# Kernel optimization log

Hardware: AMD Instinct MI355X
Metric: run time of the kernel (lower is better)

The kernel has to match this reference:

```python
import jax, jax.numpy as jnp
import numpy as np

N = 50000   # nodes
E = 800000  # edges before self-loops
H = 4       # heads
D = 64      # num_h_feats (per-head out dim of hidden layers)
C = 2       # num_classes
NEG = 0.2   # DGL GATConv leaky_relu negative_slope
EPS = 1e-5  # BatchNorm eps


def setup_inputs() -> dict:
    key = jax.random.key(0)
    ks = jax.random.split(key, 16)
    inp = {}
    inp['feats'] = jax.random.normal(ks[0], (N, 9), jnp.float32)
    inp['W1'] = jax.random.normal(ks[1], (9, H * D), jnp.float32) * 0.1
    inp['al1'] = jax.random.normal(ks[2], (H, D), jnp.float32) * 0.1
    inp['ar1'] = jax.random.normal(ks[3], (H, D), jnp.float32) * 0.1
    inp['b1'] = jnp.zeros((H, D), jnp.float32)
    inp['Wm'] = jax.random.normal(ks[4], (D, H * D), jnp.float32) * 0.1
    inp['alm'] = jax.random.normal(ks[5], (H, D), jnp.float32) * 0.1
    inp['arm'] = jax.random.normal(ks[6], (H, D), jnp.float32) * 0.1
    inp['bm'] = jnp.zeros((H, D), jnp.float32)
    inp['W2'] = jax.random.normal(ks[7], (D, H * C), jnp.float32) * 0.1
    inp['al2'] = jax.random.normal(ks[8], (H, C), jnp.float32) * 0.1
    inp['ar2'] = jax.random.normal(ks[9], (H, C), jnp.float32) * 0.1
    inp['b2'] = jnp.zeros((H, C), jnp.float32)
    inp['gamma'] = jnp.ones((D,), jnp.float32)
    inp['beta'] = jnp.zeros((D,), jnp.float32)
    inp['src'] = jax.random.randint(ks[10], (E,), 0, N, jnp.int32)
    inp['dst'] = jax.random.randint(ks[11], (E,), 0, N, jnp.int32)
    return inp


def gat_layer(x, W, al, ar, b, src, dst, out_d):
    """DGL GATConv: linear -> per-edge attention -> dst-softmax -> scatter-sum."""
    n = x.shape[0]
    z = (x @ W).reshape(n, H, out_d)                 # [N, H, Dout]
    el = jnp.sum(z * al, axis=-1)                    # [N, H] attn on src
    er = jnp.sum(z * ar, axis=-1)                    # [N, H] attn on dst
    e = jax.nn.leaky_relu(el[src] + er[dst], NEG)    # [E, H]
    m = jax.ops.segment_max(e, dst, num_segments=n)  # per-dst max (stable softmax)
    a = jnp.exp(e - m[dst])
    s = jax.ops.segment_sum(a, dst, num_segments=n)
    alpha = a / s[dst]                               # [E, H]
    out = jax.ops.segment_sum(alpha[:, :, None] * z[src], dst, num_segments=n)
    return out + b                                   # [N, H, Dout]


def batchnorm(h, gamma, beta):
    mu = jnp.mean(h, axis=0)
    var = jnp.var(h, axis=0)
    return (h - mu) * jax.lax.rsqrt(var + EPS) * gamma + beta


def reference(feats, W1, al1, ar1, b1, Wm, alm, arm, bm, W2, al2, ar2, b2,
              gamma, beta, src, dst):
    # dgl.add_self_loop
    loop = jnp.arange(N, dtype=src.dtype)
    s = jnp.concatenate([src, loop])
    d = jnp.concatenate([dst, loop])
    h = gat_layer(feats, W1, al1, ar1, b1, s, d, D).sum(axis=1)  # head-sum
    h = batchnorm(h, gamma, beta)
    h = gat_layer(h, Wm, alm, arm, bm, s, d, D).sum(axis=1)
    h = batchnorm(h, gamma, beta)
    o = gat_layer(h, W2, al2, ar2, b2, s, d, C).sum(axis=1)      # [N, C]
    return o
```

## Files before the change

kernel.cpp:

```cpp
#include <hip/hip_runtime.h>
#include <hip/hip_bf16.h>

typedef __hip_bfloat16 bf16;
typedef __bf16 bf16x8 __attribute__((ext_vector_type(8)));
typedef float f32x4 __attribute__((ext_vector_type(4)));
typedef _Float16 h16;
typedef _Float16 h16x4 __attribute__((ext_vector_type(4)));

#define LOG2E 1.44269504088896340736f

__device__ __forceinline__ float b2f(bf16 v) { return __bfloat162float(v); }

__device__ __forceinline__ float ldin(const void* p, size_t i, int isb) {
    return isb ? b2f(((const bf16*)p)[i]) : ((const float*)p)[i];
}
__device__ __forceinline__ unsigned short f2bfbits(float f) {
    bf16 v = __float2bfloat16(f);
    return *(unsigned short*)&v;
}

__global__ __launch_bounds__(256) void prep_kernel(
    const void* __restrict__ feats, const void* __restrict__ W1, const void* __restrict__ Wm,
    const void* __restrict__ al1, const void* __restrict__ ar1,
    const void* __restrict__ alm, const void* __restrict__ arm,
    const unsigned* __restrict__ gbits,
    const int* __restrict__ dstv, int* __restrict__ deg,
    unsigned short* __restrict__ fpad, unsigned short* __restrict__ W1T,
    unsigned short* __restrict__ WmT,
    float* __restrict__ alf1, float* __restrict__ arf1,
    float* __restrict__ alfm, float* __restrict__ arfm,
    unsigned short* __restrict__ zhs, float* __restrict__ zcs, float* __restrict__ elp,
    int* __restrict__ flag, int Nn, int E) {
    int isb = (gbits[0] == 0x3F803F80u) ? 1 : 0;
    long t = (long)blockIdx.x * 256 + threadIdx.x;
    if (t == 0) *flag = isb;
    long b0 = (long)Nn * 8;
    long b1 = b0 + 2048;
    long b2 = b1 + 2048;
    long b3 = b2 + 256;
    long b4 = b3 + 268;
    long b5 = b4 + E;
    if (t < b0) {
        int s = (int)(t & 7); long n = t >> 3;
        int k0 = s * 8;
        union { unsigned short us[8]; uint4 v; } o;
#pragma unroll
        for (int j = 0; j < 8; j++) {
            int k = k0 + j;
            o.us[j] = (k < 9) ? f2bfbits(ldin(feats, (size_t)n * 9 + k, isb))
                              : (unsigned short)0;
        }
        *(uint4*)(fpad + t * 8) = o.v;
    } else if (t < b1) {
        long u = t - b0;
        int col = (int)(u >> 3), k0 = ((int)u & 7) * 8;
        union { unsigned short us[8]; uint4 v; } o;
#pragma unroll
        for (int j = 0; j < 8; j++) {
            int k = k0 + j;
            o.us[j] = (k < 9) ? f2bfbits(ldin(W1, (size_t)k * 256 + col, isb))
                              : (unsigned short)0;
        }
        *(uint4*)(W1T + u * 8) = o.v;
    } else if (t < b2) {
        long u = t - b1;
        int col = (int)(u >> 3), k0 = ((int)u & 7) * 8;
        union { unsigned short us[8]; uint4 v; } o;
#pragma unroll
        for (int j = 0; j < 8; j++) {
            int k = k0 + j;
            o.us[j] = f2bfbits(ldin(Wm, (size_t)k * 256 + col, isb));
        }
        *(uint4*)(WmT + u * 8) = o.v;
    } else if (t < b3) {
        int u = (int)(t - b2);
        alf1[u] = ldin(al1, u, isb) * LOG2E; arf1[u] = ldin(ar1, u, isb) * LOG2E;
        alfm[u] = ldin(alm, u, isb) * LOG2E; arfm[u] = ldin(arm, u, isb) * LOG2E;
    } else if (t < b4) {
        long u = t - b3;
        if (u < 4) {
            elp[(size_t)Nn * 4 + u] = -1e30f;
        } else if (u < 260) {
            zhs[(size_t)Nn * 256 + (u - 4)] = 0;
        } else {
            zcs[(size_t)Nn * 8 + (u - 260)] = 0.f;
        }
    } else if (t < b5) {
        atomicAdd(&deg[dstv[t - b4]], 1);
    }
}

__global__ __launch_bounds__(256) void scan1_kernel(
    const int* __restrict__ deg, int* __restrict__ off, int* __restrict__ bsum, int Nn) {
    __shared__ int s[256];
    int t = threadIdx.x, i = blockIdx.x * 256 + t;
    int v = (i < Nn) ? ((deg[i] + 3) & ~3) : 0;
    s[t] = v; __syncthreads();
#pragma unroll
    for (int o = 1; o < 256; o <<= 1) {
        int a = (t >= o) ? s[t - o] : 0;
        __syncthreads();
        s[t] += a;
        __syncthreads();
    }
    if (i < Nn) off[i] = s[t];
    if (t == 255) bsum[blockIdx.x] = s[255];
}

__global__ __launch_bounds__(256) void scan3_kernel(
    const int* __restrict__ deg, int* __restrict__ off, int* __restrict__ cur,
    int* __restrict__ adj, const int* __restrict__ bsum, int Nn, int NB) {
    __shared__ int s[256];
    int t = threadIdx.x;
    int v = (t < NB) ? bsum[t] : 0;
    s[t] = v; __syncthreads();
#pragma unroll
    for (int o = 1; o < 256; o <<= 1) {
        int a = (t >= o) ? s[t - o] : 0;
        __syncthreads();
        s[t] += a;
        __syncthreads();
    }
    s[t] -= v;
    __syncthreads();
    int base = s[blockIdx.x];
    int i = blockIdx.x * 256 + t;
    if (i < Nn) {
        int d = deg[i], pd = (d + 3) & ~3;
        int ex = off[i] - pd + base;
        off[i] = ex;
        cur[i] = ex;
        for (int j = d; j < pd; j++) adj[ex + j] = Nn;
        if (i == Nn - 1) {
            int tot = ex + pd;
            off[Nn] = tot;
            for (int j = 0; j < 32; j++) adj[tot + j] = Nn;
        }
    }
}

__global__ __launch_bounds__(256) void scatter_kernel(
    const int* __restrict__ src, const int* __restrict__ dst,
    int* __restrict__ cur, int* __restrict__ adj, int E) {
    int t = blockIdx.x * 256 + threadIdx.x;
    if (t < E) {
        int p = atomicAdd(&cur[dst[t]], 1);
        adj[p] = src[t];
    }
}

__global__ __launch_bounds__(256) void lin_mfma_l1_kernel(
    const unsigned short* __restrict__ xb, const unsigned short* __restrict__ WT,
    const float* __restrict__ alf, const float* __restrict__ arf,
    h16* __restrict__ zh, float* __restrict__ el, float* __restrict__ er, int Nn) {
    __shared__ h16 zs[16 * 256];
    int w = threadIdx.x >> 6;
    int l = threadIdx.x & 63;
    int quad = l >> 4, lc = l & 15;
    int node0 = blockIdx.x * 16;

    int mrow = node0 + lc; if (mrow >= Nn) mrow = Nn - 1;
    const bf16x8* xa = (const bf16x8*)(xb + (size_t)mrow * 64);
    bf16x8 a0 = xa[quad];
    bf16x8 a1 = xa[quad + 4];

    float pe[4] = {0.f, 0.f, 0.f, 0.f}, pr[4] = {0.f, 0.f, 0.f, 0.f};
    int row0 = quad * 4;
#pragma unroll
    for (int ct = 0; ct < 4; ++ct) {
        int col = w * 64 + ct * 16 + lc;
        const bf16x8* wb = (const bf16x8*)(WT + (size_t)col * 64);
        bf16x8 b0 = wb[quad];
        bf16x8 b1 = wb[quad + 4];
        f32x4 c = {0.f, 0.f, 0.f, 0.f};
        c = __builtin_amdgcn_mfma_f32_16x16x32_bf16(a0, b0, c, 0, 0, 0);
        c = __builtin_amdgcn_mfma_f32_16x16x32_bf16(a1, b1, c, 0, 0, 0);
        float av = alf[col], rv = arf[col];
#pragma unroll
        for (int r = 0; r < 4; ++r) {
            pe[r] = fmaf(c[r], av, pe[r]);
            pr[r] = fmaf(c[r], rv, pr[r]);
            zs[(row0 + r) * 256 + col] = (h16)c[r];
        }
    }
#pragma unroll
    for (int o = 1; o < 16; o <<= 1) {
#pragma unroll
        for (int r = 0; r < 4; ++r) {
            pe[r] += __shfl_xor(pe[r], o);
            pr[r] += __shfl_xor(pr[r], o);
        }
    }
    if (lc == 0) {
#pragma unroll
        for (int r = 0; r < 4; ++r) {
            int n = node0 + row0 + r;
            if (n < Nn) { el[n * 4 + w] = pe[r]; er[n * 4 + w] = pr[r]; }
        }
    }
    __syncthreads();
#pragma unroll
    for (int it = 0; it < 2; ++it) {
        int flat = it * 2048 + threadIdx.x * 8;
        int row = flat >> 8;
        if (node0 + row < Nn)
            *(uint4*)(zh + (size_t)node0 * 256 + flat) = *(const uint4*)(zs + flat);
    }
}

__global__ __launch_bounds__(256) void lin_mfma_bn_kernel(
    const float* __restrict__ x,
    const float* __restrict__ bnsum, const float* __restrict__ bnsumsq,
    const void* __restrict__ gamma, const void* __restrict__ beta,
    const unsigned short* __restrict__ WT,
    const float* __restrict__ alf, const float* __restrict__ arf,
    h16* __restrict__ zh, float* __restrict__ el, float* __restrict__ er,
    const int* __restrict__ flag, int Nn) {
    __shared__ h16 zs[16 * 256];
    __shared__ __align__(16) float scs[64], shs[64];
    int tid = threadIdx.x;
    if (tid < 64) {
        int isb = *flag;
        float inv_n = 1.f / (float)Nn;
        float mu = bnsum[tid] * inv_n;
        float var = bnsumsq[tid] * inv_n - mu * mu;
        float s = rsqrtf(var + 1e-5f) * ldin(gamma, tid, isb);
        scs[tid] = s;
        shs[tid] = ldin(beta, tid, isb) - mu * s;
    }
    __syncthreads();

    int w = tid >> 6;
    int l = tid & 63;
    int quad = l >> 4, lc = l & 15;
    int node0 = blockIdx.x * 16;

    int mrow = node0 + lc; if (mrow >= Nn) mrow = Nn - 1;
    const float* xr = x + (size_t)mrow * 64 + quad * 8;
    float4 f0 = ((const float4*)xr)[0];
    float4 f1 = ((const float4*)xr)[1];
    float4 f2 = ((const float4*)(xr + 32))[0];
    float4 f3 = ((const float4*)(xr + 32))[1];
    float4 s0 = ((const float4*)(scs + quad * 8))[0];
    float4 s1 = ((const float4*)(scs + quad * 8))[1];
    float4 s2 = ((const float4*)(scs + 32 + quad * 8))[0];
    float4 s3 = ((const float4*)(scs + 32 + quad * 8))[1];
    float4 h0 = ((const float4*)(shs + quad * 8))[0];
    float4 h1 = ((const float4*)(shs + quad * 8))[1];
    float4 h2 = ((const float4*)(shs + 32 + quad * 8))[0];
    float4 h3 = ((const float4*)(shs + 32 + quad * 8))[1];

    union { bf16x8 v; unsigned short s[8]; } ua, ub;
    ua.s[0] = f2bfbits(fmaf(f0.x, s0.x, h0.x));
    ua.s[1] = f2bfbits(fmaf(f0.y, s0.y, h0.y));
    ua.s[2] = f2bfbits(fmaf(f0.z, s0.z, h0.z));
    ua.s[3] = f2bfbits(fmaf(f0.w, s0.w, h0.w));
    ua.s[4] = f2bfbits(fmaf(f1.x, s1.x, h1.x));
    ua.s[5] = f2bfbits(fmaf(f1.y, s1.y, h1.y));
    ua.s[6] = f2bfbits(fmaf(f1.z, s1.z, h1.z));
    ua.s[7] = f2bfbits(fmaf(f1.w, s1.w, h1.w));
    ub.s[0] = f2bfbits(fmaf(f2.x, s2.x, h2.x));
    ub.s[1] = f2bfbits(fmaf(f2.y, s2.y, h2.y));
    ub.s[2] = f2bfbits(fmaf(f2.z, s2.z, h2.z));
    ub.s[3] = f2bfbits(fmaf(f2.w, s2.w, h2.w));
    ub.s[4] = f2bfbits(fmaf(f3.x, s3.x, h3.x));
    ub.s[5] = f2bfbits(fmaf(f3.y, s3.y, h3.y));
    ub.s[6] = f2bfbits(fmaf(f3.z, s3.z, h3.z));
    ub.s[7] = f2bfbits(fmaf(f3.w, s3.w, h3.w));
    bf16x8 a0 = ua.v, a1 = ub.v;

    float pe[4] = {0.f, 0.f, 0.f, 0.f}, pr[4] = {0.f, 0.f, 0.f, 0.f};
    int row0 = quad * 4;
#pragma unroll
    for (int ct = 0; ct < 4; ++ct) {
        int col = w * 64 + ct * 16 + lc;
        const bf16x8* wb = (const bf16x8*)(WT + (size_t)col * 64);
        bf16x8 b0 = wb[quad];
        bf16x8 b1 = wb[quad + 4];
        f32x4 c = {0.f, 0.f, 0.f, 0.f};
        c = __builtin_amdgcn_mfma_f32_16x16x32_bf16(a0, b0, c, 0, 0, 0);
        c = __builtin_amdgcn_mfma_f32_16x16x32_bf16(a1, b1, c, 0, 0, 0);
        float av = alf[col], rv = arf[col];
#pragma unroll
        for (int r = 0; r < 4; ++r) {
            pe[r] = fmaf(c[r], av, pe[r]);
            pr[r] = fmaf(c[r], rv, pr[r]);
            zs[(row0 + r) * 256 + col] = (h16)c[r];
        }
    }
#pragma unroll
    for (int o = 1; o < 16; o <<= 1) {
#pragma unroll
        for (int r = 0; r < 4; ++r) {
            pe[r] += __shfl_xor(pe[r], o);
            pr[r] += __shfl_xor(pr[r], o);
        }
    }
    if (lc == 0) {
#pragma unroll
        for (int r = 0; r < 4; ++r) {
            int n = node0 + row0 + r;
            if (n < Nn) { el[n * 4 + w] = pe[r]; er[n * 4 + w] = pr[r]; }
        }
    }
    __syncthreads();
#pragma unroll
    for (int it = 0; it < 2; ++it) {
        int flat = it * 2048 + threadIdx.x * 8;
        int row = flat >> 8;
        if (node0 + row < Nn)
            *(uint4*)(zh + (size_t)node0 * 256 + flat) = *(const uint4*)(zs + flat);
    }
}

__global__ __launch_bounds__(256) void bnstats_kernel(
    const float* __restrict__ x, float* __restrict__ bnsum, float* __restrict__ bnsumsq,
    int Nn) {
    __shared__ float ssum[4][64], ssq[4][64];
    int tid = threadIdx.x;
    int d = tid & 63, r = tid >> 6;
    float s = 0.f, q = 0.f;
    int stride = gridDim.x * 4;
    for (int n = blockIdx.x * 4 + r; n < Nn; n += stride) {
        float v = x[(size_t)n * 64 + d];
        s += v;
        q = fmaf(v, v, q);
    }
    ssum[r][d] = s; ssq[r][d] = q;
    __syncthreads();
    if (tid < 64) {
        float ts = ssum[0][tid] + ssum[1][tid] + ssum[2][tid] + ssum[3][tid];
        float tq = ssq[0][tid] + ssq[1][tid] + ssq[2][tid] + ssq[3][tid];
        atomicAdd(&bnsum[tid], ts);
        atomicAdd(&bnsumsq[tid], tq);
    }
}

__global__ __launch_bounds__(256) void lin3_kernel(
    const float* __restrict__ x,
    const float* __restrict__ bnsum, const float* __restrict__ bnsumsq,
    const void* __restrict__ gamma, const void* __restrict__ beta,
    const void* __restrict__ W, const void* __restrict__ al, const void* __restrict__ ar,
    float* __restrict__ zc, float* __restrict__ el, float* __restrict__ er,
    const int* __restrict__ flag, int Nn) {
    __shared__ __align__(16) float scs[64], shs[64];
    int isb = *flag;
    int tid = threadIdx.x;
    if (tid < 64) {
        float inv_n = 1.f / (float)Nn;
        float mu = bnsum[tid] * inv_n;
        float var = bnsumsq[tid] * inv_n - mu * mu;
        float s = rsqrtf(var + 1e-5f) * ldin(gamma, tid, isb);
        scs[tid] = s;
        shs[tid] = ldin(beta, tid, isb) - mu * s;
    }
    __syncthreads();
    int t = blockIdx.x * 256 + tid;
    if (t >= Nn * 4) return;
    int n = t >> 2, h = t & 3;
    const float4* xr4 = (const float4*)(x + (size_t)n * 64);
    float a0 = 0.f, a1 = 0.f;
#pragma unroll 4
    for (int kk = 0; kk < 16; kk++) {
        float4 xv = xr4[kk];
        int k = kk * 4;
        float xn;
        xn = fmaf(xv.x, scs[k + 0], shs[k + 0]);
        a0 += xn * ldin(W, (k + 0) * 8 + h * 2, isb);
        a1 += xn * ldin(W, (k + 0) * 8 + h * 2 + 1, isb);
        xn = fmaf(xv.y, scs[k + 1], shs[k + 1]);
        a0 += xn * ldin(W, (k + 1) * 8 + h * 2, isb);
        a1 += xn * ldin(W, (k + 1) * 8 + h * 2 + 1, isb);
        xn = fmaf(xv.z, scs[k + 2], shs[k + 2]);
        a0 += xn * ldin(W, (k + 2) * 8 + h * 2, isb);
        a1 += xn * ldin(W, (k + 2) * 8 + h * 2 + 1, isb);
        xn = fmaf(xv.w, scs[k + 3], shs[k + 3]);
        a0 += xn * ldin(W, (k + 3) * 8 + h * 2, isb);
        a1 += xn * ldin(W, (k + 3) * 8 + h * 2 + 1, isb);
    }
    zc[n * 8 + h * 2 + 0] = a0;
    zc[n * 8 + h * 2 + 1] = a1;
    el[t] = (a0 * ldin(al, h * 2, isb) + a1 * ldin(al, h * 2 + 1, isb)) * LOG2E;
    er[t] = (a0 * ldin(ar, h * 2, isb) + a1 * ldin(ar, h * 2 + 1, isb)) * LOG2E;
}

#define GATH(ev, zv, sv)                                        \
    {                                                           \
        ev[0] = el[sv.x * 4 + h]; ev[1] = el[sv.y * 4 + h];     \
        ev[2] = el[sv.z * 4 + h]; ev[3] = el[sv.w * 4 + h];     \
        zv[0] = zrow[(size_t)sv.x * 64 + l];                    \
        zv[1] = zrow[(size_t)sv.y * 64 + l];                    \
        zv[2] = zrow[(size_t)sv.z * 64 + l];                    \
        zv[3] = zrow[(size_t)sv.w * 64 + l];                    \
    }
#define COMP(ev, zv)                                        \
    {                                                       \
        _Pragma("unroll") for (int j = 0; j < 4; j++) {     \
            float e = ev[j] + ern;                          \
            e = fmaxf(e, 0.2f * e);                         \
            float wj = __builtin_amdgcn_exp2f(e);           \
            lsum += wj;                                     \
            acc.x = fmaf(wj, (float)zv[j].x, acc.x);        \
            acc.y = fmaf(wj, (float)zv[j].y, acc.y);        \
            acc.z = fmaf(wj, (float)zv[j].z, acc.z);        \
            acc.w = fmaf(wj, (float)zv[j].w, acc.w);        \
        }                                                   \
    }

__global__ __launch_bounds__(256) void gat_agg64_kernel(
    const h16* __restrict__ zh, const float* __restrict__ el, const float* __restrict__ er,
    const int* __restrict__ off, const int* __restrict__ adj, const void* __restrict__ bias,
    float* __restrict__ x, const int* __restrict__ flag, int Nn, int total_waves) {
    int isb = *flag;
    int tid = threadIdx.x;
    int l = tid & 63;
    int h = l >> 4;
    int gw = blockIdx.x * 4 + (tid >> 6);
    const h16x4* zrow = (const h16x4*)zh;

    float4 bsl;
    bsl.x = ldin(bias, l * 4 + 0, isb);
    bsl.y = ldin(bias, l * 4 + 1, isb);
    bsl.z = ldin(bias, l * 4 + 2, isb);
    bsl.w = ldin(bias, l * 4 + 3, isb);

    if (gw >= Nn) return;

    int n = gw;
    int fs0 = off[n], fs1 = off[n + 1];
    float fel = el[n * 4 + h], fer = er[n * 4 + h];
    int4 fsv = *(const int4*)(adj + fs0);

    while (true) {
        int s0 = fs0;
        int nb = (fs1 - fs0) >> 2;
        float eln = fel, ern = fer;
        int4 svA = fsv;
        h16x4 zself = zrow[(size_t)n * 64 + l];
        int nn = n + total_waves;
        if (nn < Nn) {
            fs0 = off[nn]; fs1 = off[nn + 1];
            fel = el[nn * 4 + h]; fer = er[nn * 4 + h];
            fsv = *(const int4*)(adj + fs0);
        }

        float e0 = eln + ern;
        e0 = fmaxf(e0, 0.2f * e0);
        float w0 = __builtin_amdgcn_exp2f(e0);
        float lsum = w0;
        float4 acc = {0.f, 0.f, 0.f, 0.f};

        if (nb > 0) {
            float evA[4], evB[4], evC[4];
            h16x4 zvA[4], zvB[4], zvC[4];
            GATH(evA, zvA, svA);
            int4 svB = *(const int4*)(adj + s0 + 4);
            if (nb > 1) GATH(evB, zvB, svB);
            int4 svC = *(const int4*)(adj + s0 + 8);
            int k = 0;
            while (true) {
                if (k + 2 < nb) GATH(evC, zvC, svC);
                svA = *(const int4*)(adj + s0 + (k + 3) * 4);
                COMP(evA, zvA);
                if (++k >= nb) break;
                if (k + 2 < nb) GATH(evA, zvA, svA);
                svB = *(const int4*)(adj + s0 + (k + 3) * 4);
                COMP(evB, zvB);
                if (++k >= nb) break;
                if (k + 2 < nb) GATH(evB, zvB, svB);
                svC = *(const int4*)(adj + s0 + (k + 3) * 4);
                COMP(evC, zvC);
                if (++k >= nb) break;
            }
        }

        acc.x = fmaf(w0, (float)zself.x, acc.x);
        acc.y = fmaf(w0, (float)zself.y, acc.y);
        acc.z = fmaf(w0, (float)zself.z, acc.z);
        acc.w = fmaf(w0, (float)zself.w, acc.w);

        float inv = 1.f / lsum;
        float4 r;
        r.x = fmaf(acc.x, inv, bsl.x);
        r.y = fmaf(acc.y, inv, bsl.y);
        r.z = fmaf(acc.z, inv, bsl.z);
        r.w = fmaf(acc.w, inv, bsl.w);
#pragma unroll
        for (int o = 16; o < 64; o <<= 1) {
            r.x += __shfl_xor(r.x, o);
            r.y += __shfl_xor(r.y, o);
            r.z += __shfl_xor(r.z, o);
            r.w += __shfl_xor(r.w, o);
        }
        if (h == 0) ((float4*)(x + (size_t)n * 64))[l & 15] = r;
        if (nn >= Nn) break;
        n = nn;
    }
}
#undef GATH
#undef COMP

#define GATH2(ev, zv, sv)                                       \
    {                                                           \
        ev[0] = el[sv.x * 4 + h]; zv[0] = zc2[sv.x * 4 + h];    \
        ev[1] = el[sv.y * 4 + h]; zv[1] = zc2[sv.y * 4 + h];    \
        ev[2] = el[sv.z * 4 + h]; zv[2] = zc2[sv.z * 4 + h];    \
        ev[3] = el[sv.w * 4 + h]; zv[3] = zc2[sv.w * 4 + h];    \
    }
#define COMP2(ev, zv)                                       \
    {                                                       \
        _Pragma("unroll") for (int j = 0; j < 4; j++) {     \
            float e = ev[j] + er_nh;                        \
            e = fmaxf(e, 0.2f * e);                         \
            float w = __builtin_amdgcn_exp2f(e);            \
            lsum += w;                                      \
            a0 = fmaf(w, zv[j].x, a0);                      \
            a1 = fmaf(w, zv[j].y, a1);                      \
        }                                                   \
    }

__global__ __launch_bounds__(256) void gat_agg2_kernel(
    const float* __restrict__ zc, const float* __restrict__ el, const float* __restrict__ er,
    const int* __restrict__ off, const int* __restrict__ adj, const void* __restrict__ bias,
    void* __restrict__ out, const int* __restrict__ flag, int Nn) {
    int isb = *flag;
    int t = blockIdx.x * 256 + threadIdx.x;
    if (t >= Nn * 4) return;
    int n = t >> 2, h = t & 3;
    const float2* zc2 = (const float2*)zc;
    float er_nh = er[n * 4 + h];
    float e0 = el[n * 4 + h] + er_nh;
    e0 = fmaxf(e0, 0.2f * e0);
    float w0 = __builtin_amdgcn_exp2f(e0);
    float lsum = w0;
    float2 zn = zc2[n * 4 + h];
    float a0 = w0 * zn.x, a1 = w0 * zn.y;
    int s0 = off[n];
    int nb = (off[n + 1] - s0) >> 2;
    if (nb > 0) {
        float evA[4], evB[4], evC[4];
        float2 zvA[4], zvB[4], zvC[4];
        int4 svA = *(const int4*)(adj + s0);
        GATH2(evA, zvA, svA);
        int4 svB = *(const int4*)(adj + s0 + 4);
        if (nb > 1) GATH2(evB, zvB, svB);
        int4 svC = *(const int4*)(adj + s0 + 8);
        int k = 0;
        while (true) {
            if (k + 2 < nb) GATH2(evC, zvC, svC);
            svA = *(const int4*)(adj + s0 + (k + 3) * 4);
            COMP2(evA, zvA);
            if (++k >= nb) break;
            if (k + 2 < nb) GATH2(evA, zvA, svA);
            svB = *(const int4*)(adj + s0 + (k + 3) * 4);
            COMP2(evB, zvB);
            if (++k >= nb) break;
            if (k + 2 < nb) GATH2(evB, zvB, svB);
            svC = *(const int4*)(adj + s0 + (k + 3) * 4);
            COMP2(evC, zvC);
            if (++k >= nb) break;
        }
    }
    float inv = 1.f / lsum;
    float v0 = fmaf(a0, inv, ldin(bias, h * 2 + 0, isb));
    float v1 = fmaf(a1, inv, ldin(bias, h * 2 + 1, isb));
#pragma unroll
    for (int o = 1; o < 4; o <<= 1) {
        v0 += __shfl_xor(v0, o);
        v1 += __shfl_xor(v1, o);
    }
    if (h == 0) {
        if (isb) {
            ((bf16*)out)[n * 2 + 0] = __float2bfloat16(v0);
            ((bf16*)out)[n * 2 + 1] = __float2bfloat16(v1);
        } else {
            ((float*)out)[n * 2 + 0] = v0;
            ((float*)out)[n * 2 + 1] = v1;
        }
    }
}
#undef GATH2
#undef COMP2

extern "C" void kernel_launch(void* const* d_in, const int* in_sizes, int n_in,
                              void* d_out, int out_size, void* d_ws, size_t ws_size,
                              hipStream_t stream) {
    const void* feats = d_in[0];
    const void* W1    = d_in[1];
    const void* al1   = d_in[2];
    const void* ar1   = d_in[3];
    const void* b1    = d_in[4];
    const void* Wm    = d_in[5];
    const void* alm   = d_in[6];
    const void* arm   = d_in[7];
    const void* bm    = d_in[8];
    const void* W2    = d_in[9];
    const void* al2   = d_in[10];
    const void* ar2   = d_in[11];
    const void* b2v   = d_in[12];
    const void* gamma = d_in[13];
    const void* beta  = d_in[14];
    const int*  src   = (const int*)d_in[15];
    const int*  dst   = (const int*)d_in[16];

    int Nn = in_sizes[0] / 9;
    int E  = in_sizes[15];

    float* ws = (float*)d_ws;
    h16*   zh   = (h16*)ws;
    float* zc   = ws + (size_t)(Nn + 1) * 128;
    float* el   = zc + (size_t)Nn * 8 + 8;
    float* er   = el + (size_t)Nn * 4 + 4;
    float* x    = er + (size_t)Nn * 4;
    int*   deg  = (int*)(x + (size_t)Nn * 64);
    float* bns1 = (float*)(deg + Nn);
    float* bnq1 = bns1 + 64;
    float* bns2 = bnq1 + 64;
    float* bnq2 = bns2 + 64;
    size_t msetBytes = (size_t)Nn * 4 + 256 * 4;
    float* alf1 = bnq2 + 64;
    float* arf1 = alf1 + 256;
    float* alfm = arf1 + 256;
    float* arfm = alfm + 256;
    unsigned short* fpad =
        (unsigned short*)(((uintptr_t)(arfm + 256) + 15) & ~(uintptr_t)15);
    unsigned short* W1T  = fpad + (size_t)Nn * 64;
    unsigned short* WmT  = W1T + 256 * 64;
    int*   flag = (int*)(WmT + 256 * 64);
    int*   off  = flag + 1;
    int*   cur  = off + Nn + 1;
    int*   adj  = (int*)(((uintptr_t)(cur + Nn) + 15) & ~(uintptr_t)15);
    int*   bsum = adj + E + 3 * Nn + 32;

    dim3 B(256);
    int NB1 = (Nn + 255) / 256;
    int gE  = (E + 255) / 256;
    int gMF = (Nn + 15) / 16;
    int gN4 = (Nn * 4 + 255) / 256;
    long prepN = (long)Nn * 8 + 2048 + 2048 + 256 + 268 + E;
    int gPrep = (int)((prepN + 255) / 256);
    int AGG_GRID = 4096;
    int total_waves = AGG_GRID * 4;

    hipMemsetAsync(deg, 0, msetBytes, stream);

    prep_kernel<<<gPrep, B, 0, stream>>>(feats, W1, Wm, al1, ar1, alm, arm,
                                         (const unsigned*)gamma, dst, deg,
                                         fpad, W1T, WmT,
                                         alf1, arf1, alfm, arfm,
                                         (unsigned short*)zh, zc, el, flag, Nn, E);

    scan1_kernel<<<NB1, B, 0, stream>>>(deg, off, bsum, Nn);
    scan3_kernel<<<NB1, B, 0, stream>>>(deg, off, cur, adj, bsum, Nn, NB1);
    scatter_kernel<<<gE, B, 0, stream>>>(src, dst, cur, adj, E);

    lin_mfma_l1_kernel<<<gMF, B, 0, stream>>>(fpad, W1T, alf1, arf1, zh, el, er, Nn);
    gat_agg64_kernel<<<AGG_GRID, B, 0, stream>>>(
        zh, el, er, off, adj, b1, x, flag, Nn, total_waves);
    bnstats_kernel<<<512, B, 0, stream>>>(x, bns1, bnq1, Nn);

    lin_mfma_bn_kernel<<<gMF, B, 0, stream>>>(x, bns1, bnq1, gamma, beta,
                                              WmT, alfm, arfm, zh, el, er, flag, Nn);
    gat_agg64_kernel<<<AGG_GRID, B, 0, stream>>>(
        zh, el, er, off, adj, bm, x, flag, Nn, total_waves);
    bnstats_kernel<<<512, B, 0, stream>>>(x, bns2, bnq2, Nn);

    lin3_kernel<<<gN4, B, 0, stream>>>(x, bns2, bnq2, gamma, beta,
                                       W2, al2, ar2, zc, el, er, flag, Nn);
    gat_agg2_kernel<<<gN4, B, 0, stream>>>(zc, el, er, off, adj, b2v, d_out, flag, Nn);
}
```

Baseline: 448.8 us.

## Fuse BN statistics into GAT aggregation and read raw feats in layer-1 matmul

Batch-norm sum and sum-of-squares are now accumulated inside the aggregation kernel, per wave, then reduced through shared memory and atomics. This removes the two separate bnstats passes that re-read x. The layer-1 linear kernel now converts the 9-wide feats directly into bf16 and issues one MFMA instead of two, so the padded fpad buffer and its prep stage are gone. The aggregation grid is halved and the gather prefetch depth drops from three stages to two, which lowers register pressure but leaves less memory latency hidden.

New measurement: 469.8 us. 4.7% more time.

```diff
diff --git a/kernel.cpp b/kernel.cpp
--- a/kernel.cpp
+++ b/kernel.cpp
@@ -20,13 +20,12 @@
 }
 
 __global__ __launch_bounds__(256) void prep_kernel(
-    const void* __restrict__ feats, const void* __restrict__ W1, const void* __restrict__ Wm,
+    const void* __restrict__ W1, const void* __restrict__ Wm,
     const void* __restrict__ al1, const void* __restrict__ ar1,
     const void* __restrict__ alm, const void* __restrict__ arm,
     const unsigned* __restrict__ gbits,
     const int* __restrict__ dstv, int* __restrict__ deg,
-    unsigned short* __restrict__ fpad, unsigned short* __restrict__ W1T,
-    unsigned short* __restrict__ WmT,
+    unsigned short* __restrict__ W1T, unsigned short* __restrict__ WmT,
     float* __restrict__ alf1, float* __restrict__ arf1,
     float* __restrict__ alfm, float* __restrict__ arfm,
     unsigned short* __restrict__ zhs, float* __restrict__ zcs, float* __restrict__ elp,
@@ -34,23 +33,22 @@
     int isb = (gbits[0] == 0x3F803F80u) ? 1 : 0;
     long t = (long)blockIdx.x * 256 + threadIdx.x;
     if (t == 0) *flag = isb;
-    long b0 = (long)Nn * 8;
+    long b0 = 2048;
     long b1 = b0 + 2048;
-    long b2 = b1 + 2048;
-    long b3 = b2 + 256;
-    long b4 = b3 + 268;
-    long b5 = b4 + E;
+    long b2 = b1 + 256;
+    long b3 = b2 + 268;
+    long b4 = b3 + E;
     if (t < b0) {
-        int s = (int)(t & 7); long n = t >> 3;
-        int k0 = s * 8;
+        long u = t;
+        int col = (int)(u >> 3), k0 = ((int)u & 7) * 8;
         union { unsigned short us[8]; uint4 v; } o;
 #pragma unroll
         for (int j = 0; j < 8; j++) {
             int k = k0 + j;
-            o.us[j] = (k < 9) ? f2bfbits(ldin(feats, (size_t)n * 9 + k, isb))
+            o.us[j] = (k < 9) ? f2bfbits(ldin(W1, (size_t)k * 256 + col, isb))
                               : (unsigned short)0;
         }
-        *(uint4*)(fpad + t * 8) = o.v;
+        *(uint4*)(W1T + u * 8) = o.v;
     } else if (t < b1) {
         long u = t - b0;
         int col = (int)(u >> 3), k0 = ((int)u & 7) * 8;
@@ -58,26 +56,15 @@
 #pragma unroll
         for (int j = 0; j < 8; j++) {
             int k = k0 + j;
-            o.us[j] = (k < 9) ? f2bfbits(ldin(W1, (size_t)k * 256 + col, isb))
-                              : (unsigned short)0;
-        }
-        *(uint4*)(W1T + u * 8) = o.v;
+            o.us[j] = f2bfbits(ldin(Wm, (size_t)k * 256 + col, isb));
+        }
+        *(uint4*)(WmT + u * 8) = o.v;
     } else if (t < b2) {
-        long u = t - b1;
-        int col = (int)(u >> 3), k0 = ((int)u & 7) * 8;
-        union { unsigned short us[8]; uint4 v; } o;
-#pragma unroll
-        for (int j = 0; j < 8; j++) {
-            int k = k0 + j;
-            o.us[j] = f2bfbits(ldin(Wm, (size_t)k * 256 + col, isb));
-        }
-        *(uint4*)(WmT + u * 8) = o.v;
-    } else if (t < b3) {
-        int u = (int)(t - b2);
+        int u = (int)(t - b1);
         alf1[u] = ldin(al1, u, isb) * LOG2E; arf1[u] = ldin(ar1, u, isb) * LOG2E;
         alfm[u] = ldin(alm, u, isb) * LOG2E; arfm[u] = ldin(arm, u, isb) * LOG2E;
-    } else if (t < b4) {
-        long u = t - b3;
+    } else if (t < b3) {
+        long u = t - b2;
         if (u < 4) {
             elp[(size_t)Nn * 4 + u] = -1e30f;
         } else if (u < 260) {
@@ -85,8 +72,8 @@
         } else {
             zcs[(size_t)Nn * 8 + (u - 260)] = 0.f;
         }
-    } else if (t < b5) {
-        atomicAdd(&deg[dstv[t - b4]], 1);
+    } else if (t < b4) {
+        atomicAdd(&deg[dstv[t - b3]], 1);
     }
 }
 
@@ -150,19 +137,26 @@
 }
 
 __global__ __launch_bounds__(256) void lin_mfma_l1_kernel(
-    const unsigned short* __restrict__ xb, const unsigned short* __restrict__ WT,
+    const void* __restrict__ feats, const unsigned short* __restrict__ WT,
     const float* __restrict__ alf, const float* __restrict__ arf,
-    h16* __restrict__ zh, float* __restrict__ el, float* __restrict__ er, int Nn) {
+    h16* __restrict__ zh, float* __restrict__ el, float* __restrict__ er,
+    const int* __restrict__ flag, int Nn) {
     __shared__ h16 zs[16 * 256];
+    int isb = *flag;
     int w = threadIdx.x >> 6;
     int l = threadIdx.x & 63;
     int quad = l >> 4, lc = l & 15;
     int node0 = blockIdx.x * 16;
 
     int mrow = node0 + lc; if (mrow >= Nn) mrow = Nn - 1;
-    const bf16x8* xa = (const bf16x8*)(xb + (size_t)mrow * 64);
-    bf16x8 a0 = xa[quad];
-    bf16x8 a1 = xa[quad + 4];
+    union { unsigned short s[8]; bf16x8 v; } ua;
+#pragma unroll
+    for (int j = 0; j < 8; j++) {
+        int k = quad * 8 + j;
+        ua.s[j] = (k < 9) ? f2bfbits(ldin(feats, (size_t)mrow * 9 + k, isb))
+                          : (unsigned short)0;
+    }
+    bf16x8 a0 = ua.v;
 
     float pe[4] = {0.f, 0.f, 0.f, 0.f}, pr[4] = {0.f, 0.f, 0.f, 0.f};
     int row0 = quad * 4;
@@ -171,10 +165,8 @@
         int col = w * 64 + ct * 16 + lc;
         const bf16x8* wb = (const bf16x8*)(WT + (size_t)col * 64);
         bf16x8 b0 = wb[quad];
-        bf16x8 b1 = wb[quad + 4];
         f32x4 c = {0.f, 0.f, 0.f, 0.f};
         c = __builtin_amdgcn_mfma_f32_16x16x32_bf16(a0, b0, c, 0, 0, 0);
-        c = __builtin_amdgcn_mfma_f32_16x16x32_bf16(a1, b1, c, 0, 0, 0);
         float av = alf[col], rv = arf[col];
 #pragma unroll
         for (int r = 0; r < 4; ++r) {
@@ -310,29 +302,6 @@
         int row = flat >> 8;
         if (node0 + row < Nn)
             *(uint4*)(zh + (size_t)node0 * 256 + flat) = *(const uint4*)(zs + flat);
-    }
-}
-
-__global__ __launch_bounds__(256) void bnstats_kernel(
-    const float* __restrict__ x, float* __restrict__ bnsum, float* __restrict__ bnsumsq,
-    int Nn) {
-    __shared__ float ssum[4][64], ssq[4][64];
-    int tid = threadIdx.x;
-    int d = tid & 63, r = tid >> 6;
-    float s = 0.f, q = 0.f;
-    int stride = gridDim.x * 4;
-    for (int n = blockIdx.x * 4 + r; n < Nn; n += stride) {
-        float v = x[(size_t)n * 64 + d];
-        s += v;
-        q = fmaf(v, v, q);
-    }
-    ssum[r][d] = s; ssq[r][d] = q;
-    __syncthreads();
-    if (tid < 64) {
-        float ts = ssum[0][tid] + ssum[1][tid] + ssum[2][tid] + ssum[3][tid];
-        float tq = ssq[0][tid] + ssq[1][tid] + ssq[2][tid] + ssq[3][tid];
-        atomicAdd(&bnsum[tid], ts);
-        atomicAdd(&bnsumsq[tid], tq);
     }
 }
 
@@ -410,12 +379,15 @@
 __global__ __launch_bounds__(256) void gat_agg64_kernel(
     const h16* __restrict__ zh, const float* __restrict__ el, const float* __restrict__ er,
     const int* __restrict__ off, const int* __restrict__ adj, const void* __restrict__ bias,
-    float* __restrict__ x, const int* __restrict__ flag, int Nn, int total_waves) {
+    float* __restrict__ x, float* __restrict__ bnsum, float* __restrict__ bnsumsq,
+    const int* __restrict__ flag, int Nn, int total_waves) {
+    __shared__ __align__(16) float s_sum[4][64], s_sq[4][64];
     int isb = *flag;
     int tid = threadIdx.x;
+    int wv = tid >> 6;
     int l = tid & 63;
     int h = l >> 4;
-    int gw = blockIdx.x * 4 + (tid >> 6);
+    int gw = blockIdx.x * 4 + wv;
     const h16x4* zrow = (const h16x4*)zh;
 
     float4 bsl;
@@ -424,7 +396,7 @@
     bsl.z = ldin(bias, l * 4 + 2, isb);
     bsl.w = ldin(bias, l * 4 + 3, isb);
 
-    if (gw >= Nn) return;
+    float4 bs = {0.f, 0.f, 0.f, 0.f}, bq = {0.f, 0.f, 0.f, 0.f};
 
     int n = gw;
     int fs0 = off[n], fs1 = off[n + 1];
@@ -451,25 +423,19 @@
         float4 acc = {0.f, 0.f, 0.f, 0.f};
 
         if (nb > 0) {
-            float evA[4], evB[4], evC[4];
-            h16x4 zvA[4], zvB[4], zvC[4];
+            float evA[4], evB[4];
+            h16x4 zvA[4], zvB[4];
             GATH(evA, zvA, svA);
             int4 svB = *(const int4*)(adj + s0 + 4);
-            if (nb > 1) GATH(evB, zvB, svB);
-            int4 svC = *(const int4*)(adj + s0 + 8);
             int k = 0;
             while (true) {
-                if (k + 2 < nb) GATH(evC, zvC, svC);
-                svA = *(const int4*)(adj + s0 + (k + 3) * 4);
+                if (k + 1 < nb) GATH(evB, zvB, svB);
+                svA = *(const int4*)(adj + s0 + (k + 2) * 4);
                 COMP(evA, zvA);
                 if (++k >= nb) break;
-                if (k + 2 < nb) GATH(evA, zvA, svA);
-                svB = *(const int4*)(adj + s0 + (k + 3) * 4);
+                if (k + 1 < nb) GATH(evA, zvA, svA);
+                svB = *(const int4*)(adj + s0 + (k + 2) * 4);
                 COMP(evB, zvB);
-                if (++k >= nb) break;
-                if (k + 2 < nb) GATH(evB, zvB, svB);
-                svC = *(const int4*)(adj + s0 + (k + 3) * 4);
-                COMP(evC, zvC);
                 if (++k >= nb) break;
             }
         }
@@ -492,9 +458,25 @@
             r.z += __shfl_xor(r.z, o);
             r.w += __shfl_xor(r.w, o);
         }
-        if (h == 0) ((float4*)(x + (size_t)n * 64))[l & 15] = r;
+        if (h == 0) {
+            ((float4*)(x + (size_t)n * 64))[l & 15] = r;
+            bs.x += r.x; bs.y += r.y; bs.z += r.z; bs.w += r.w;
+            bq.x = fmaf(r.x, r.x, bq.x); bq.y = fmaf(r.y, r.y, bq.y);
+            bq.z = fmaf(r.z, r.z, bq.z); bq.w = fmaf(r.w, r.w, bq.w);
+        }
         if (nn >= Nn) break;
         n = nn;
+    }
+    if (h == 0) {
+        ((float4*)&s_sum[wv][0])[l & 15] = bs;
+        ((float4*)&s_sq[wv][0])[l & 15] = bq;
+    }
+    __syncthreads();
+    if (tid < 64) {
+        float ts = s_sum[0][tid] + s_sum[1][tid] + s_sum[2][tid] + s_sum[3][tid];
+        float tq = s_sq[0][tid] + s_sq[1][tid] + s_sq[2][tid] + s_sq[3][tid];
+        atomicAdd(&bnsum[tid], ts);
+        atomicAdd(&bnsumsq[tid], tq);
     }
 }
 #undef GATH
@@ -622,9 +604,8 @@
     float* arf1 = alf1 + 256;
     float* alfm = arf1 + 256;
     float* arfm = alfm + 256;
-    unsigned short* fpad =
+    unsigned short* W1T =
         (unsigned short*)(((uintptr_t)(arfm + 256) + 15) & ~(uintptr_t)15);
-    unsigned short* W1T  = fpad + (size_t)Nn * 64;
     unsigned short* WmT  = W1T + 256 * 64;
     int*   flag = (int*)(WmT + 256 * 64);
     int*   off  = flag + 1;
@@ -637,16 +618,16 @@
     int gE  = (E + 255) / 256;
     int gMF = (Nn + 15) / 16;
     int gN4 = (Nn * 4 + 255) / 256;
-    long prepN = (long)Nn * 8 + 2048 + 2048 + 256 + 268 + E;
+    long prepN = 2048 + 2048 + 256 + 268 + (long)E;
     int gPrep = (int)((prepN + 255) / 256);
-    int AGG_GRID = 4096;
+    int AGG_GRID = 2048;
     int total_waves = AGG_GRID * 4;
 
     hipMemsetAsync(deg, 0, msetBytes, stream);
 
-    prep_kernel<<<gPrep, B, 0, stream>>>(feats, W1, Wm, al1, ar1, alm, arm,
+    prep_kernel<<<gPrep, B, 0, stream>>>(W1, Wm, al1, ar1, alm, arm,
                                          (const unsigned*)gamma, dst, deg,
-                                         fpad, W1T, WmT,
+                                         W1T, WmT,
                                          alf1, arf1, alfm, arfm,
                                          (unsigned short*)zh, zc, el, flag, Nn, E);
 
@@ -654,16 +635,15 @@
     scan3_kernel<<<NB1, B, 0, stream>>>(deg, off, cur, adj, bsum, Nn, NB1);
     scatter_kernel<<<gE, B, 0, stream>>>(src, dst, cur, adj, E);
 
-    lin_mfma_l1_kernel<<<gMF, B, 0, stream>>>(fpad, W1T, alf1, arf1, zh, el, er, Nn);
+    lin_mfma_l1_kernel<<<gMF, B, 0, stream>>>(feats, W1T, alf1, arf1,
+                                              zh, el, er, flag, Nn);
     gat_agg64_kernel<<<AGG_GRID, B, 0, stream>>>(
-        zh, el, er, off, adj, b1, x, flag, Nn, total_waves);
-    bnstats_kernel<<<512, B, 0, stream>>>(x, bns1, bnq1, Nn);
+        zh, el, er, off, adj, b1, x, bns1, bnq1, flag, Nn, total_waves);
 
     lin_mfma_bn_kernel<<<gMF, B, 0, stream>>>(x, bns1, bnq1, gamma, beta,
                                               WmT, alfm, arfm, zh, el, er, flag, Nn);
     gat_agg64_kernel<<<AGG_GRID, B, 0, stream>>>(
-        zh, el, er, off, adj, bm, x, flag, Nn, total_waves);
-    bnstats_kernel<<<512, B, 0, stream>>>(x, bns2, bnq2, Nn);
+        zh, el, er, off, adj, bm, x, bns2, bnq2, flag, Nn, total_waves);
 
     lin3_kernel<<<gN4, B, 0, stream>>>(x, bns2, bnq2, gamma, beta,
                                        W2, al2, ar2, zc, el, er, flag, Nn);
```
